# Optimization experiments

Measured on AMD Instinct MI355X. Metric: run time of the kernel, lower is better.

Reference implementation:

```python
import jax, jax.numpy as jnp
import numpy as np

NUM_HEADS = 8


def _nearest_idx(x, x_grid):
    # x: [b,n,dx]; x_grid: [b,H,W,dx] regular grid -> flat nearest cell index [b,n]
    b = x.shape[0]
    H, W = x_grid.shape[1], x_grid.shape[2]
    gf = x_grid.reshape(b, H * W, -1)
    lo = gf[:, :1]   # min corner [b,1,dx]
    hi = gf[:, -1:]  # max corner [b,1,dx]
    dims = jnp.asarray([H, W], dtype=x.dtype)
    t = (x - lo) / (hi - lo) * (dims - 1.0)
    idx = jnp.clip(jnp.round(t), 0.0, dims - 1.0).astype(jnp.int32)  # [b,n,2]
    return idx[..., 0] * W + idx[..., 1]


def _cumcount(idx):
    # per-batch cumulative count of each value, in order of appearance
    b, n = idx.shape
    order = jnp.argsort(idx, axis=1, stable=True)
    s = jnp.take_along_axis(idx, order, axis=1)
    ar = jnp.arange(n)
    new_run = jnp.concatenate([jnp.ones((b, 1), bool), s[:, 1:] != s[:, :-1]], axis=1)
    run_start = jax.lax.cummax(jnp.where(new_run, ar, 0), axis=1)
    cc_sorted = (ar - run_start).astype(jnp.int32)
    return jnp.zeros((b, n), jnp.int32).at[jnp.arange(b)[:, None], order].set(cc_sorted)


def _mhca(q_in, kv, mask, Wq, Wk, Wv, Wo):
    # q_in: [B,1,e]; kv: [B,K,e]; mask: [B,K] (True = attend)
    B, K, e = kv.shape
    dh = e // NUM_HEADS
    q = (q_in @ Wq).reshape(B, 1, NUM_HEADS, dh)
    k = (kv @ Wk).reshape(B, K, NUM_HEADS, dh)
    v = (kv @ Wv).reshape(B, K, NUM_HEADS, dh)
    scores = jnp.einsum('bqhd,bkhd->bhqk', q, k) / jnp.sqrt(jnp.asarray(dh, q.dtype))
    scores = jnp.where(mask[:, None, None, :], scores, jnp.finfo(scores.dtype).min)
    attn = jax.nn.softmax(scores, axis=-1)
    out = jnp.einsum('bhqk,bkhd->bqhd', attn, v).reshape(B, 1, e)
    return out @ Wo


def setup_inputs() -> dict:
    key = jax.random.key(0)
    ks = jax.random.split(key, 8)
    b, n, e, H, W = 8, 8192, 128, 64, 64
    x = jax.random.uniform(ks[0], (b, n, 2), jnp.float32)
    z = jax.random.normal(ks[1], (b, n, e), jnp.float32)
    g0 = jnp.linspace(0.0, 1.0, H)
    g1 = jnp.linspace(0.0, 1.0, W)
    mg = jnp.stack(jnp.meshgrid(g0, g1, indexing='ij'), axis=-1)  # [H,W,2]
    x_grid = jnp.broadcast_to(mg, (b, H, W, 2)).astype(jnp.float32)
    z_grid = jax.random.normal(ks[2], (b, H, W, e), jnp.float32)
    latent = jax.random.normal(ks[3], (e,), jnp.float32)
    scale = 1.0 / np.sqrt(e).astype(np.float32)
    Wq = jax.random.normal(ks[4], (e, e), jnp.float32) * scale
    Wk = jax.random.normal(ks[5], (e, e), jnp.float32) * scale
    Wv = jax.random.normal(ks[6], (e, e), jnp.float32) * scale
    Wo = jax.random.normal(ks[7], (e, e), jnp.float32) * scale
    return {"x": x, "z": z, "x_grid": x_grid, "z_grid": z_grid, "latent": latent,
            "Wq": Wq, "Wk": Wk, "Wv": Wv, "Wo": Wo, "max_patch": 20}


def reference(x, z, x_grid, z_grid, latent, Wq, Wk, Wv, Wo, max_patch):
    b, n, e = z.shape
    H, W = x_grid.shape[1], x_grid.shape[2]
    S = H * W
    nearest = _nearest_idx(x, x_grid)                    # [b,n]
    cc = _cumcount(nearest)                              # [b,n]
    bidx = jnp.broadcast_to(jnp.arange(b)[:, None], (b, n))
    valid = cc < max_patch
    slot = jnp.where(valid, cc, 0)
    # ragged scatter: pack each point's z into its grid cell's padded sequence
    joint = jnp.zeros((b, S, max_patch, e), z.dtype)
    joint = joint.at[bidx, nearest, slot].add(z * valid[..., None].astype(z.dtype))
    zg_flat = z_grid.reshape(b, S, e)
    joint = jnp.concatenate([joint, zg_flat[:, :, None, :]], axis=2)  # [b,S,P+1,e]
    counts = jnp.zeros((b, S), jnp.int32).at[bidx, nearest].add(1)
    mask = jnp.arange(max_patch + 1)[None, None, :] < jnp.minimum(counts, max_patch)[..., None]
    mask = mask.at[..., -1].set(True)  # grid token always attended
    joint = joint.reshape(b * S, max_patch + 1, e)
    mask = mask.reshape(b * S, max_patch + 1)
    q = jnp.broadcast_to(latent, (b * S, 1, e))          # z0_grid queries
    zg = _mhca(q, joint, mask, Wq, Wk, Wv, Wo)           # [b*S,1,e]
    zg = zg.reshape(b, H, W, e)
    return x_grid, zg
```

## Files before the change

kernel.cpp:

```cpp
#include <hip/hip_runtime.h>
#include <cstdint>
#include <cstddef>

#define S_CELLS 4096
#define NB      8
#define NPTS    8192
#define E       128
#define MAXP    20
#define NHEADS  8
#define NPT_ROWS 65536
#define NGR_ROWS 32768

#define WS_COUNTS 0
#define WS_SLOTS  131072
#define WS_WT1    2752512
#define WS_WT2    2793472
#define WS_SC     2828288
#define WS_V      5974016

typedef __attribute__((ext_vector_type(8))) short bf16x8;
typedef __attribute__((ext_vector_type(4))) float f32x4;

__device__ __forceinline__ unsigned short f2bf_bits(float f) {
    unsigned u = __float_as_uint(f);
    unsigned rounded = u + 0x7FFFu + ((u >> 16) & 1u);
    return (unsigned short)(rounded >> 16);
}
__device__ __forceinline__ unsigned short f2bf_rta(float f) {
    return (unsigned short)((__float_as_uint(f) + 0x8000u) >> 16);
}
__device__ __forceinline__ unsigned pack_bf2(float a, float b) {
    unsigned ua = __float_as_uint(a) + 0x8000u;
    unsigned ub = __float_as_uint(b) + 0x8000u;
    return (ua >> 16) | (ub & 0xFFFF0000u);
}
__device__ __forceinline__ float bf2f(unsigned short u) {
    return __uint_as_float(((unsigned)u) << 16);
}

__global__ void __launch_bounds__(256)
k_prep(const float* __restrict__ latent,
       const float* __restrict__ Wq,
       const float* __restrict__ Wk,
       const float* __restrict__ Wv,
       const float* __restrict__ Wo,
       int* __restrict__ counts,
       unsigned short* __restrict__ WT1,
       unsigned short* __restrict__ WT2) {
    const int t   = threadIdx.x;
    const int blk = blockIdx.x;

    {
        int4* c4 = (int4*)counts;
        for (int idx = blk * 256 + t; idx < 8192; idx += 9 * 256)
            c4[idx] = int4{0, 0, 0, 0};
    }

    if (blk == 0) {
        __shared__ float lat[E];
        __shared__ float qv[E];
        const int j = t & 127;
        if (t < E) lat[t] = latent[t];
        __syncthreads();
        float acc = 0.0f;
        for (int k2 = 0; k2 < E; ++k2) acc += lat[k2] * Wq[k2 * E + j];
        qv[j] = acc;
        __syncthreads();
        const int hb = (t >> 7) * 4;
        for (int h = hb; h < hb + 4; ++h) {
            float a = 0.0f;
            #pragma unroll
            for (int d = 0; d < 16; ++d) a += Wk[j * E + h * 16 + d] * qv[h * 16 + d];
            WT1[(size_t)(128 + h) * 136 + j] = f2bf_bits(a * 0.25f);
        }
        for (int idx = t; idx < 8 * 136; idx += 256) {
            int rr = idx / 136, cc = idx - rr * 136;
            WT1[(size_t)(136 + rr) * 136 + cc] = 0;
        }
        return;
    }

    const float* W = (blk < 5) ? Wv : Wo;
    unsigned short* WT = (blk < 5) ? WT1 : WT2;
    const int n0 = ((blk - 1) & 3) * 32;
    __shared__ float lbuf[128][33];
    #pragma unroll
    for (int it = 0; it < 16; ++it) {
        int k  = (t >> 5) + it * 8;
        int nl = t & 31;
        lbuf[k][nl] = W[(size_t)k * E + n0 + nl];
    }
    __syncthreads();
    for (int idx = t; idx < 32 * 136; idx += 256) {
        int nl = idx / 136, k = idx - nl * 136;
        float v = (k < 128) ? lbuf[k][nl] : 0.0f;
        WT[(size_t)(n0 + nl) * 136 + k] = f2bf_bits(v);
    }
}

__device__ __forceinline__ bf16x8 load_afrag_f32(const float* __restrict__ X,
                                                 int row, int kq, int q) {
    const float4* xr = (const float4*)(X + (size_t)row * E);
    float4 lo = xr[kq * 8 + q * 2];
    float4 hi = xr[kq * 8 + q * 2 + 1];
    unsigned u[4];
    u[0] = pack_bf2(lo.x, lo.y);
    u[1] = pack_bf2(lo.z, lo.w);
    u[2] = pack_bf2(hi.x, hi.y);
    u[3] = pack_bf2(hi.z, hi.w);
    union { unsigned u4[4]; bf16x8 v; } cv;
    cv.u4[0] = u[0]; cv.u4[1] = u[1]; cv.u4[2] = u[2]; cv.u4[3] = u[3];
    return cv.v;
}

__global__ void __launch_bounds__(256)
k_main(const float* __restrict__ x,
       const float* __restrict__ x_grid,
       const float* __restrict__ Xz,
       const float* __restrict__ Xg,
       const unsigned short* __restrict__ WT1g,
       int* __restrict__ counts,
       int* __restrict__ slots,
       unsigned short* __restrict__ V,
       float* __restrict__ SC,
       float* __restrict__ out_xgrid) {
    __shared__ unsigned short W_t[20480];

    const int t = threadIdx.x;

    if (blockIdx.x >= 768) {
        int i = (blockIdx.x - 768) * 256 + t;
        out_xgrid[i] = x_grid[i];
        int b = i >> 13;
        float x0 = x[(size_t)i * 2 + 0];
        float x1 = x[(size_t)i * 2 + 1];
        int i0 = (int)rintf(x0 * 63.0f);
        int i1 = (int)rintf(x1 * 63.0f);
        i0 = min(max(i0, 0), 63);
        i1 = min(max(i1, 0), 63);
        int cell = b * S_CELLS + i0 * 64 + i1;
        int slot = atomicAdd(&counts[cell], 1);
        if (slot < MAXP) slots[(size_t)cell * MAXP + slot] = i & (NPTS - 1);
        return;
    }

    {
        const float4* src = (const float4*)WT1g;
        float4* dst = (float4*)W_t;
        #pragma unroll
        for (int it = 0; it < 10; ++it) dst[t + it * 256] = src[t + it * 256];
    }
    __syncthreads();

    const int lane = t & 63;
    const int wv   = t >> 6;
    const int cn   = lane & 15;
    const int q    = lane >> 4;

    const int grow0 = blockIdx.x * 128;
    const float* Xsrc;
    int srow;
    if (blockIdx.x < 512) { Xsrc = Xz; srow = grow0; }
    else                  { Xsrc = Xg; srow = grow0 - NPT_ROWS; }

    f32x4 acc[2][9];
    #pragma unroll
    for (int mt = 0; mt < 2; ++mt)
        #pragma unroll
        for (int nt = 0; nt < 9; ++nt)
            acc[mt][nt] = f32x4{0.0f, 0.0f, 0.0f, 0.0f};

    #pragma unroll
    for (int kq = 0; kq < 4; ++kq) {
        bf16x8 a[2];
        #pragma unroll
        for (int mt = 0; mt < 2; ++mt)
            a[mt] = load_afrag_f32(Xsrc, srow + wv * 32 + mt * 16 + cn, kq, q);
        #pragma unroll
        for (int nt = 0; nt < 9; ++nt) {
            const bf16x8 b = *(const bf16x8*)&W_t[(size_t)(nt * 16 + cn) * 136 + kq * 32 + q * 8];
            #pragma unroll
            for (int mt = 0; mt < 2; ++mt)
                acc[mt][nt] = __builtin_amdgcn_mfma_f32_16x16x32_bf16(
                    a[mt], b, acc[mt][nt], 0, 0, 0);
        }
    }

    #pragma unroll
    for (int mt = 0; mt < 2; ++mt) {
        const int rb = grow0 + wv * 32 + mt * 16 + q * 4;
        #pragma unroll
        for (int nt = 0; nt < 8; ++nt)
            #pragma unroll
            for (int r = 0; r < 4; ++r)
                V[(size_t)(rb + r) * E + nt * 16 + cn] = f2bf_rta(acc[mt][nt][r]);
        if (cn < 8) {
            #pragma unroll
            for (int r = 0; r < 4; ++r)
                SC[(size_t)(rb + r) * NHEADS + cn] = acc[mt][8][r];
        }
    }
}

__global__ void __launch_bounds__(1024)
k_attn_proj(const int* __restrict__ counts,
            const int* __restrict__ slots,
            const float* __restrict__ SC,
            const unsigned short* __restrict__ Vg,
            const unsigned short* __restrict__ WT2g,
            float* __restrict__ zg) {
    __shared__ __align__(16) unsigned short X_s[16][136];

    const int t    = threadIdx.x;
    const int lane = t & 63;
    const int wv   = t >> 6;
    const int cb   = blockIdx.x * 16;
    const int b    = cb >> 12;
    const int base = b * NPTS;
    const int cn   = lane & 15;
    const int q    = lane >> 4;

    bf16x8 bfr[4];
    if (wv < 8) {
        #pragma unroll
        for (int kq = 0; kq < 4; ++kq)
            bfr[kq] = *(const bf16x8*)&WT2g[(size_t)(wv * 16 + cn) * 136 + kq * 32 + q * 8];
    }

    const int cell = cb + wv;
    const int m    = min(counts[cell], MAXP);
    int sl = (lane < MAXP) ? slots[(size_t)cell * MAXP + lane] : 0;
    const int h = lane >> 3;

    size_t r0 = (size_t)(NPT_ROWS + cell);
    float mm = SC[r0 * NHEADS + h];
    float ss = 1.0f;
    unsigned v0 = *(const unsigned*)(Vg + r0 * E + 2 * lane);
    float o0 = bf2f((unsigned short)v0);
    float o1 = bf2f((unsigned short)(v0 >> 16));

    for (int t0 = 0; t0 < m; t0 += 4) {
        float av[4], p0[4], p1[4];
        #pragma unroll
        for (int j = 0; j < 4; ++j) {
            int pt = __shfl(sl, t0 + j, 64);
            bool val = (t0 + j) < m;
            pt = val ? pt : 0;
            size_t r = (size_t)(base + pt);
            float sa = SC[r * NHEADS + h];
            av[j] = val ? sa : -1e30f;
            unsigned vv = *(const unsigned*)(Vg + r * E + 2 * lane);
            p0[j] = bf2f((unsigned short)vv);
            p1[j] = bf2f((unsigned short)(vv >> 16));
        }
        #pragma unroll
        for (int j = 0; j < 4; ++j) {
            float nm = fmaxf(mm, av[j]);
            float e  = __expf(av[j] - nm);
            float al = __expf(mm - nm);
            ss = ss * al + e;
            o0 = o0 * al + e * p0[j];
            o1 = o1 * al + e * p1[j];
            mm = nm;
        }
    }
    float inv = 1.0f / ss;
    *(unsigned*)&X_s[wv][2 * lane] = pack_bf2(o0 * inv, o1 * inv);
    __syncthreads();

    if (wv < 8) {
        f32x4 acc = f32x4{0.0f, 0.0f, 0.0f, 0.0f};
        #pragma unroll
        for (int kq = 0; kq < 4; ++kq) {
            bf16x8 a = *(const bf16x8*)&X_s[cn][kq * 32 + q * 8];
            acc = __builtin_amdgcn_mfma_f32_16x16x32_bf16(a, bfr[kq], acc, 0, 0, 0);
        }
        #pragma unroll
        for (int r = 0; r < 4; ++r)
            zg[(size_t)(cb + q * 4 + r) * E + wv * 16 + cn] = acc[r];
    }
}

extern "C" void kernel_launch(void* const* d_in, const int* in_sizes, int n_in,
                              void* d_out, int out_size, void* d_ws, size_t ws_size,
                              hipStream_t stream) {
    const float* x      = (const float*)d_in[0];
    const float* z      = (const float*)d_in[1];
    const float* x_grid = (const float*)d_in[2];
    const float* z_grid = (const float*)d_in[3];
    const float* latent = (const float*)d_in[4];
    const float* Wq     = (const float*)d_in[5];
    const float* Wk     = (const float*)d_in[6];
    const float* Wv     = (const float*)d_in[7];
    const float* Wo     = (const float*)d_in[8];

    char* ws = (char*)d_ws;
    int*            counts = (int*)(ws + WS_COUNTS);
    int*            slots  = (int*)(ws + WS_SLOTS);
    unsigned short* WT1    = (unsigned short*)(ws + WS_WT1);
    unsigned short* WT2    = (unsigned short*)(ws + WS_WT2);
    float*          SC     = (float*)(ws + WS_SC);
    unsigned short* V      = (unsigned short*)(ws + WS_V);

    float* out_xgrid = (float*)d_out;
    float* zg        = (float*)d_out + NB * NPTS;

    k_prep<<<9, 256, 0, stream>>>(latent, Wq, Wk, Wv, Wo, counts, WT1, WT2);

    k_main<<<1024, 256, 0, stream>>>(x, x_grid, z, z_grid, WT1,
                                     counts, slots, V, SC, out_xgrid);

    k_attn_proj<<<2048, 1024, 0, stream>>>(counts, slots, SC, V, WT2, zg);
}
```

Measured before the change: 137.0 us.

## Fuse weight prep into main kernel and bin points per batch in shared memory

Removes the separate prep kernel launch. Each GEMM block now builds its own bf16 transposed Wv tile and the folded q·Wk rows in shared memory, and a few extra blocks prepare WT2 and copy x_grid with float4 stores. Point binning becomes one block per batch using shared-memory atomic counters and writes counts at the end, so the global count zeroing and global atomics go away. The trade-off is redundant per-block weight conversion and the q projection, plus serialised binning over 8192 points in each of 8 blocks, which may sit on the critical path.

```diff
diff --git a/kernel.cpp b/kernel.cpp
--- a/kernel.cpp
+++ b/kernel.cpp
@@ -13,7 +13,6 @@
 
 #define WS_COUNTS 0
 #define WS_SLOTS  131072
-#define WS_WT1    2752512
 #define WS_WT2    2793472
 #define WS_SC     2828288
 #define WS_V      5974016
@@ -34,68 +33,11 @@
     unsigned ub = __float_as_uint(b) + 0x8000u;
     return (ua >> 16) | (ub & 0xFFFF0000u);
 }
+__device__ __forceinline__ unsigned pack_bf2_rne(float a, float b) {
+    return ((unsigned)f2bf_bits(a)) | (((unsigned)f2bf_bits(b)) << 16);
+}
 __device__ __forceinline__ float bf2f(unsigned short u) {
     return __uint_as_float(((unsigned)u) << 16);
-}
-
-__global__ void __launch_bounds__(256)
-k_prep(const float* __restrict__ latent,
-       const float* __restrict__ Wq,
-       const float* __restrict__ Wk,
-       const float* __restrict__ Wv,
-       const float* __restrict__ Wo,
-       int* __restrict__ counts,
-       unsigned short* __restrict__ WT1,
-       unsigned short* __restrict__ WT2) {
-    const int t   = threadIdx.x;
-    const int blk = blockIdx.x;
-
-    {
-        int4* c4 = (int4*)counts;
-        for (int idx = blk * 256 + t; idx < 8192; idx += 9 * 256)
-            c4[idx] = int4{0, 0, 0, 0};
-    }
-
-    if (blk == 0) {
-        __shared__ float lat[E];
-        __shared__ float qv[E];
-        const int j = t & 127;
-        if (t < E) lat[t] = latent[t];
-        __syncthreads();
-        float acc = 0.0f;
-        for (int k2 = 0; k2 < E; ++k2) acc += lat[k2] * Wq[k2 * E + j];
-        qv[j] = acc;
-        __syncthreads();
-        const int hb = (t >> 7) * 4;
-        for (int h = hb; h < hb + 4; ++h) {
-            float a = 0.0f;
-            #pragma unroll
-            for (int d = 0; d < 16; ++d) a += Wk[j * E + h * 16 + d] * qv[h * 16 + d];
-            WT1[(size_t)(128 + h) * 136 + j] = f2bf_bits(a * 0.25f);
-        }
-        for (int idx = t; idx < 8 * 136; idx += 256) {
-            int rr = idx / 136, cc = idx - rr * 136;
-            WT1[(size_t)(136 + rr) * 136 + cc] = 0;
-        }
-        return;
-    }
-
-    const float* W = (blk < 5) ? Wv : Wo;
-    unsigned short* WT = (blk < 5) ? WT1 : WT2;
-    const int n0 = ((blk - 1) & 3) * 32;
-    __shared__ float lbuf[128][33];
-    #pragma unroll
-    for (int it = 0; it < 16; ++it) {
-        int k  = (t >> 5) + it * 8;
-        int nl = t & 31;
-        lbuf[k][nl] = W[(size_t)k * E + n0 + nl];
-    }
-    __syncthreads();
-    for (int idx = t; idx < 32 * 136; idx += 256) {
-        int nl = idx / 136, k = idx - nl * 136;
-        float v = (k < 128) ? lbuf[k][nl] : 0.0f;
-        WT[(size_t)(n0 + nl) * 136 + k] = f2bf_bits(v);
-    }
 }
 
 __device__ __forceinline__ bf16x8 load_afrag_f32(const float* __restrict__ X,
@@ -114,41 +56,109 @@
 }
 
 __global__ void __launch_bounds__(256)
-k_main(const float* __restrict__ x,
-       const float* __restrict__ x_grid,
-       const float* __restrict__ Xz,
-       const float* __restrict__ Xg,
-       const unsigned short* __restrict__ WT1g,
-       int* __restrict__ counts,
-       int* __restrict__ slots,
-       unsigned short* __restrict__ V,
-       float* __restrict__ SC,
-       float* __restrict__ out_xgrid) {
-    __shared__ unsigned short W_t[20480];
-
-    const int t = threadIdx.x;
-
-    if (blockIdx.x >= 768) {
-        int i = (blockIdx.x - 768) * 256 + t;
-        out_xgrid[i] = x_grid[i];
-        int b = i >> 13;
-        float x0 = x[(size_t)i * 2 + 0];
-        float x1 = x[(size_t)i * 2 + 1];
-        int i0 = (int)rintf(x0 * 63.0f);
-        int i1 = (int)rintf(x1 * 63.0f);
-        i0 = min(max(i0, 0), 63);
-        i1 = min(max(i1, 0), 63);
-        int cell = b * S_CELLS + i0 * 64 + i1;
-        int slot = atomicAdd(&counts[cell], 1);
-        if (slot < MAXP) slots[(size_t)cell * MAXP + slot] = i & (NPTS - 1);
+k_fused(const float* __restrict__ x,
+        const float* __restrict__ x_grid,
+        const float* __restrict__ Xz,
+        const float* __restrict__ Xg,
+        const float* __restrict__ latent,
+        const float* __restrict__ Wq,
+        const float* __restrict__ Wk,
+        const float* __restrict__ Wv,
+        const float* __restrict__ Wo,
+        int* __restrict__ counts,
+        int* __restrict__ slots,
+        unsigned short* __restrict__ V,
+        float* __restrict__ SC,
+        unsigned short* __restrict__ WT2,
+        float* __restrict__ out_xgrid) {
+    __shared__ __align__(16) char smem[40192];
+    const int t   = threadIdx.x;
+    const int blk = blockIdx.x;
+
+    if (blk >= 768) {
+        if (blk < 776) {
+            int* lcnt = (int*)smem;
+            const int b = blk - 768;
+            for (int i = t; i < S_CELLS; i += 256) lcnt[i] = 0;
+            __syncthreads();
+            const float2* xp = (const float2*)x;
+            const size_t base = (size_t)b * NPTS;
+            #pragma unroll 2
+            for (int r = 0; r < NPTS; r += 256) {
+                int p = r + t;
+                float2 xv = xp[base + p];
+                int i0 = (int)rintf(xv.x * 63.0f);
+                int i1 = (int)rintf(xv.y * 63.0f);
+                i0 = min(max(i0, 0), 63);
+                i1 = min(max(i1, 0), 63);
+                int cl = i0 * 64 + i1;
+                int slot = atomicAdd(&lcnt[cl], 1);
+                if (slot < MAXP)
+                    slots[(size_t)(b * S_CELLS + cl) * MAXP + slot] = p;
+            }
+            __syncthreads();
+            for (int i = t; i < S_CELLS; i += 256)
+                counts[b * S_CELLS + i] = lcnt[i];
+        } else if (blk < 780) {
+            float (*lbuf)[33] = (float(*)[33])smem;
+            const int n0 = (blk - 776) * 32;
+            #pragma unroll
+            for (int it = 0; it < 16; ++it) {
+                int k  = (t >> 5) + it * 8;
+                int nl = t & 31;
+                lbuf[k][nl] = Wo[(size_t)k * E + n0 + nl];
+            }
+            __syncthreads();
+            for (int idx = t; idx < 32 * 136; idx += 256) {
+                int nl = idx / 136, k = idx - nl * 136;
+                float v = (k < 128) ? lbuf[k][nl] : 0.0f;
+                WT2[(size_t)(n0 + nl) * 136 + k] = f2bf_bits(v);
+            }
+        } else {
+            int idx = (blk - 780) * 256 + t;
+            ((float4*)out_xgrid)[idx] = ((const float4*)x_grid)[idx];
+        }
         return;
     }
 
+    unsigned short* W_t = (unsigned short*)smem;
+    float* lat = (float*)(smem + 39168);
+    float* qv  = (float*)(smem + 39680);
+
+    if (t < E) lat[t] = latent[t];
+
+    #pragma unroll 8
+    for (int it = 0; it < 32; ++it) {
+        int idx = t + it * 256;
+        int kp  = idx >> 7;
+        int n   = idx & 127;
+        float a = Wv[(size_t)(2 * kp)     * E + n];
+        float b = Wv[(size_t)(2 * kp + 1) * E + n];
+        *(unsigned*)&W_t[(size_t)n * 136 + 2 * kp] = pack_bf2_rne(a, b);
+    }
+    for (int idx = t; idx < 8 * 136; idx += 256) {
+        int rr = idx / 136, cc = idx - rr * 136;
+        W_t[(size_t)(136 + rr) * 136 + cc] = 0;
+    }
+    __syncthreads();
+
+    if (t < E) {
+        float acc = 0.0f;
+        for (int k2 = 0; k2 < E; ++k2) acc += lat[k2] * Wq[k2 * E + t];
+        qv[t] = acc;
+    }
+    __syncthreads();
+
     {
-        const float4* src = (const float4*)WT1g;
-        float4* dst = (float4*)W_t;
-        #pragma unroll
-        for (int it = 0; it < 10; ++it) dst[t + it * 256] = src[t + it * 256];
+        const int j  = t & 127;
+        const int hb = (t >> 7) * 4;
+        for (int h = hb; h < hb + 4; ++h) {
+            float a = 0.0f;
+            #pragma unroll
+            for (int d = 0; d < 16; ++d)
+                a += Wk[j * E + h * 16 + d] * qv[h * 16 + d];
+            W_t[(size_t)(128 + h) * 136 + j] = f2bf_bits(a * 0.25f);
+        }
     }
     __syncthreads();
 
@@ -157,11 +167,11 @@
     const int cn   = lane & 15;
     const int q    = lane >> 4;
 
-    const int grow0 = blockIdx.x * 128;
+    const int grow0 = blk * 128;
     const float* Xsrc;
     int srow;
-    if (blockIdx.x < 512) { Xsrc = Xz; srow = grow0; }
-    else                  { Xsrc = Xg; srow = grow0 - NPT_ROWS; }
+    if (blk < 512) { Xsrc = Xz; srow = grow0; }
+    else           { Xsrc = Xg; srow = grow0 - NPT_ROWS; }
 
     f32x4 acc[2][9];
     #pragma unroll
@@ -297,7 +307,6 @@
     char* ws = (char*)d_ws;
     int*            counts = (int*)(ws + WS_COUNTS);
     int*            slots  = (int*)(ws + WS_SLOTS);
-    unsigned short* WT1    = (unsigned short*)(ws + WS_WT1);
     unsigned short* WT2    = (unsigned short*)(ws + WS_WT2);
     float*          SC     = (float*)(ws + WS_SC);
     unsigned short* V      = (unsigned short*)(ws + WS_V);
@@ -305,10 +314,9 @@
     float* out_xgrid = (float*)d_out;
     float* zg        = (float*)d_out + NB * NPTS;
 
-    k_prep<<<9, 256, 0, stream>>>(latent, Wq, Wk, Wv, Wo, counts, WT1, WT2);
-
-    k_main<<<1024, 256, 0, stream>>>(x, x_grid, z, z_grid, WT1,
-                                     counts, slots, V, SC, out_xgrid);
+    k_fused<<<844, 256, 0, stream>>>(x, x_grid, z, z_grid, latent,
+                                     Wq, Wk, Wv, Wo,
+                                     counts, slots, V, SC, WT2, out_xgrid);
 
     k_attn_proj<<<2048, 1024, 0, stream>>>(counts, slots, SC, V, WT2, zg);
 }
```

Measured after the change: 156.4 us. 1.14x slower.

## Defer V projection: aggregate raw z per head, then project after attention

Applied to the files above, without the earlier changes.

The main kernel now computes only the attention score columns instead of also projecting every point and grid row through Wv and storing a bf16 V buffer. The attention kernel gathers raw fp32 z rows, forms per-head softmax-weighted sums of them, and applies the Wv projection per head with MFMA on the aggregated rows before the Wo projection. This removes the large V write and read, at the cost of reading fp32 z (twice the bytes per gathered row), eight per-head accumulators per lane, and an extra matmul stage per cell. The online softmax is also replaced by a two-pass max/sum over at most 21 tokens.

```diff
diff --git a/kernel.cpp b/kernel.cpp
--- a/kernel.cpp
+++ b/kernel.cpp
@@ -16,7 +16,6 @@
 #define WS_WT1    2752512
 #define WS_WT2    2793472
 #define WS_SC     2828288
-#define WS_V      5974016
 
 typedef __attribute__((ext_vector_type(8))) short bf16x8;
 typedef __attribute__((ext_vector_type(4))) float f32x4;
@@ -33,9 +32,6 @@
     unsigned ua = __float_as_uint(a) + 0x8000u;
     unsigned ub = __float_as_uint(b) + 0x8000u;
     return (ua >> 16) | (ub & 0xFFFF0000u);
-}
-__device__ __forceinline__ float bf2f(unsigned short u) {
-    return __uint_as_float(((unsigned)u) << 16);
 }
 
 __global__ void __launch_bounds__(256)
@@ -121,10 +117,9 @@
        const unsigned short* __restrict__ WT1g,
        int* __restrict__ counts,
        int* __restrict__ slots,
-       unsigned short* __restrict__ V,
        float* __restrict__ SC,
        float* __restrict__ out_xgrid) {
-    __shared__ unsigned short W_t[20480];
+    __shared__ __align__(16) unsigned short sA[16 * 136];
 
     const int t = threadIdx.x;
 
@@ -145,10 +140,9 @@
     }
 
     {
-        const float4* src = (const float4*)WT1g;
-        float4* dst = (float4*)W_t;
-        #pragma unroll
-        for (int it = 0; it < 10; ++it) dst[t + it * 256] = src[t + it * 256];
+        const float4* src = (const float4*)(WT1g + 128 * 136);
+        float4* dst = (float4*)sA;
+        if (t < 272) dst[t] = src[t];
     }
     __syncthreads();
 
@@ -163,121 +157,140 @@
     if (blockIdx.x < 512) { Xsrc = Xz; srow = grow0; }
     else                  { Xsrc = Xg; srow = grow0 - NPT_ROWS; }
 
-    f32x4 acc[2][9];
-    #pragma unroll
-    for (int mt = 0; mt < 2; ++mt)
-        #pragma unroll
-        for (int nt = 0; nt < 9; ++nt)
-            acc[mt][nt] = f32x4{0.0f, 0.0f, 0.0f, 0.0f};
+    f32x4 acc[2];
+    acc[0] = f32x4{0.0f, 0.0f, 0.0f, 0.0f};
+    acc[1] = f32x4{0.0f, 0.0f, 0.0f, 0.0f};
 
     #pragma unroll
     for (int kq = 0; kq < 4; ++kq) {
-        bf16x8 a[2];
-        #pragma unroll
-        for (int mt = 0; mt < 2; ++mt)
-            a[mt] = load_afrag_f32(Xsrc, srow + wv * 32 + mt * 16 + cn, kq, q);
-        #pragma unroll
-        for (int nt = 0; nt < 9; ++nt) {
-            const bf16x8 b = *(const bf16x8*)&W_t[(size_t)(nt * 16 + cn) * 136 + kq * 32 + q * 8];
-            #pragma unroll
-            for (int mt = 0; mt < 2; ++mt)
-                acc[mt][nt] = __builtin_amdgcn_mfma_f32_16x16x32_bf16(
-                    a[mt], b, acc[mt][nt], 0, 0, 0);
+        const bf16x8 b = *(const bf16x8*)&sA[cn * 136 + kq * 32 + q * 8];
+        #pragma unroll
+        for (int mt = 0; mt < 2; ++mt) {
+            bf16x8 a = load_afrag_f32(Xsrc, srow + wv * 32 + mt * 16 + cn, kq, q);
+            acc[mt] = __builtin_amdgcn_mfma_f32_16x16x32_bf16(b, a, acc[mt], 0, 0, 0);
         }
     }
 
     #pragma unroll
     for (int mt = 0; mt < 2; ++mt) {
-        const int rb = grow0 + wv * 32 + mt * 16 + q * 4;
-        #pragma unroll
-        for (int nt = 0; nt < 8; ++nt)
-            #pragma unroll
-            for (int r = 0; r < 4; ++r)
-                V[(size_t)(rb + r) * E + nt * 16 + cn] = f2bf_rta(acc[mt][nt][r]);
-        if (cn < 8) {
-            #pragma unroll
-            for (int r = 0; r < 4; ++r)
-                SC[(size_t)(rb + r) * NHEADS + cn] = acc[mt][8][r];
-        }
-    }
-}
-
-__global__ void __launch_bounds__(1024)
+        const int rb = grow0 + wv * 32 + mt * 16 + cn;
+        if (q < 2)
+            *(f32x4*)(SC + (size_t)rb * NHEADS + q * 4) = acc[mt];
+    }
+}
+
+__global__ void __launch_bounds__(512)
 k_attn_proj(const int* __restrict__ counts,
             const int* __restrict__ slots,
             const float* __restrict__ SC,
-            const unsigned short* __restrict__ Vg,
+            const float* __restrict__ Xz,
+            const float* __restrict__ Zg,
+            const unsigned short* __restrict__ WT1g,
             const unsigned short* __restrict__ WT2g,
             float* __restrict__ zg) {
+    __shared__ __align__(16) unsigned short Y_s[8][16][136];
     __shared__ __align__(16) unsigned short X_s[16][136];
 
     const int t    = threadIdx.x;
     const int lane = t & 63;
     const int wv   = t >> 6;
-    const int cb   = blockIdx.x * 16;
-    const int b    = cb >> 12;
+    const int cb   = blockIdx.x * 8;
+    const int cell = cb + wv;
+    const int b    = cell >> 12;
     const int base = b * NPTS;
     const int cn   = lane & 15;
     const int q    = lane >> 4;
 
-    bf16x8 bfr[4];
-    if (wv < 8) {
-        #pragma unroll
-        for (int kq = 0; kq < 4; ++kq)
-            bfr[kq] = *(const bf16x8*)&WT2g[(size_t)(wv * 16 + cn) * 136 + kq * 32 + q * 8];
-    }
-
-    const int cell = cb + wv;
-    const int m    = min(counts[cell], MAXP);
+    const int m = min(counts[cell], MAXP);
     int sl = (lane < MAXP) ? slots[(size_t)cell * MAXP + lane] : 0;
-    const int h = lane >> 3;
-
-    size_t r0 = (size_t)(NPT_ROWS + cell);
-    float mm = SC[r0 * NHEADS + h];
-    float ss = 1.0f;
-    unsigned v0 = *(const unsigned*)(Vg + r0 * E + 2 * lane);
-    float o0 = bf2f((unsigned short)v0);
-    float o1 = bf2f((unsigned short)(v0 >> 16));
-
-    for (int t0 = 0; t0 < m; t0 += 4) {
-        float av[4], p0[4], p1[4];
+
+    const int hh = lane & 7;
+    const int tb = lane >> 3;
+
+    float sarr[3];
+    #pragma unroll
+    for (int p = 0; p < 3; ++p) {
+        int tt = tb + 8 * p;
+        int pt = __shfl(sl, tt, 64);
+        bool isPt = tt < m;
+        bool isG  = tt == m;
+        size_t r = isG ? (size_t)(NPT_ROWS + cell)
+                       : (size_t)(base + (isPt ? pt : 0));
+        float sc = SC[r * NHEADS + hh];
+        sarr[p] = (isPt || isG) ? sc : -1e30f;
+    }
+    float mx = fmaxf(fmaxf(sarr[0], sarr[1]), sarr[2]);
+    mx = fmaxf(mx, __shfl_xor(mx, 8, 64));
+    mx = fmaxf(mx, __shfl_xor(mx, 16, 64));
+    mx = fmaxf(mx, __shfl_xor(mx, 32, 64));
+    float e0 = __expf(sarr[0] - mx);
+    float e1 = __expf(sarr[1] - mx);
+    float e2 = __expf(sarr[2] - mx);
+    float sum = e0 + e1 + e2;
+    sum += __shfl_xor(sum, 8, 64);
+    sum += __shfl_xor(sum, 16, 64);
+    sum += __shfl_xor(sum, 32, 64);
+    float inv = 1.0f / sum;
+    float wn0 = e0 * inv, wn1 = e1 * inv, wn2 = e2 * inv;
+
+    float y0[8], y1[8];
+    #pragma unroll
+    for (int h2 = 0; h2 < 8; ++h2) { y0[h2] = 0.0f; y1[h2] = 0.0f; }
+
+    const int ntok = m + 1;
+    for (int t0 = 0; t0 < ntok; t0 += 4) {
+        float wnp = (t0 < 8) ? wn0 : ((t0 < 16) ? wn1 : wn2);
+        float2 zv[4];
         #pragma unroll
         for (int j = 0; j < 4; ++j) {
-            int pt = __shfl(sl, t0 + j, 64);
-            bool val = (t0 + j) < m;
-            pt = val ? pt : 0;
-            size_t r = (size_t)(base + pt);
-            float sa = SC[r * NHEADS + h];
-            av[j] = val ? sa : -1e30f;
-            unsigned vv = *(const unsigned*)(Vg + r * E + 2 * lane);
-            p0[j] = bf2f((unsigned short)vv);
-            p1[j] = bf2f((unsigned short)(vv >> 16));
+            int tt = t0 + j;
+            int pt = __shfl(sl, tt, 64);
+            const float* zr = (tt == m)
+                ? (Zg + (size_t)cell * E)
+                : (Xz + (size_t)(base + ((tt < m) ? pt : 0)) * E);
+            zv[j] = *(const float2*)(zr + 2 * lane);
         }
         #pragma unroll
         for (int j = 0; j < 4; ++j) {
-            float nm = fmaxf(mm, av[j]);
-            float e  = __expf(av[j] - nm);
-            float al = __expf(mm - nm);
-            ss = ss * al + e;
-            o0 = o0 * al + e * p0[j];
-            o1 = o1 * al + e * p1[j];
-            mm = nm;
-        }
-    }
-    float inv = 1.0f / ss;
-    *(unsigned*)&X_s[wv][2 * lane] = pack_bf2(o0 * inv, o1 * inv);
+            int srcb = ((t0 + j) & 7) << 3;
+            #pragma unroll
+            for (int h2 = 0; h2 < 8; ++h2) {
+                float w = __shfl(wnp, srcb + h2, 64);
+                y0[h2] = fmaf(w, zv[j].x, y0[h2]);
+                y1[h2] = fmaf(w, zv[j].y, y1[h2]);
+            }
+        }
+    }
+
+    #pragma unroll
+    for (int h2 = 0; h2 < 8; ++h2)
+        *(unsigned*)&Y_s[h2][wv][2 * lane] = pack_bf2(y0[h2], y1[h2]);
     __syncthreads();
 
-    if (wv < 8) {
-        f32x4 acc = f32x4{0.0f, 0.0f, 0.0f, 0.0f};
+    {
+        f32x4 acc2 = f32x4{0.0f, 0.0f, 0.0f, 0.0f};
         #pragma unroll
         for (int kq = 0; kq < 4; ++kq) {
-            bf16x8 a = *(const bf16x8*)&X_s[cn][kq * 32 + q * 8];
-            acc = __builtin_amdgcn_mfma_f32_16x16x32_bf16(a, bfr[kq], acc, 0, 0, 0);
+            bf16x8 aY = *(const bf16x8*)&Y_s[wv][cn][kq * 32 + q * 8];
+            bf16x8 bW = *(const bf16x8*)&WT1g[(size_t)(wv * 16 + cn) * 136 + kq * 32 + q * 8];
+            acc2 = __builtin_amdgcn_mfma_f32_16x16x32_bf16(aY, bW, acc2, 0, 0, 0);
         }
         #pragma unroll
         for (int r = 0; r < 4; ++r)
-            zg[(size_t)(cb + q * 4 + r) * E + wv * 16 + cn] = acc[r];
+            X_s[q * 4 + r][wv * 16 + cn] = f2bf_rta(acc2[r]);
+    }
+    __syncthreads();
+
+    {
+        f32x4 acc3 = f32x4{0.0f, 0.0f, 0.0f, 0.0f};
+        #pragma unroll
+        for (int kq = 0; kq < 4; ++kq) {
+            bf16x8 a   = *(const bf16x8*)&X_s[cn][kq * 32 + q * 8];
+            bf16x8 bfr = *(const bf16x8*)&WT2g[(size_t)(wv * 16 + cn) * 136 + kq * 32 + q * 8];
+            acc3 = __builtin_amdgcn_mfma_f32_16x16x32_bf16(bfr, a, acc3, 0, 0, 0);
+        }
+        if (cn < 8)
+            *(f32x4*)(zg + (size_t)(cb + cn) * E + wv * 16 + q * 4) = acc3;
     }
 }
 
@@ -300,7 +313,6 @@
     unsigned short* WT1    = (unsigned short*)(ws + WS_WT1);
     unsigned short* WT2    = (unsigned short*)(ws + WS_WT2);
     float*          SC     = (float*)(ws + WS_SC);
-    unsigned short* V      = (unsigned short*)(ws + WS_V);
 
     float* out_xgrid = (float*)d_out;
     float* zg        = (float*)d_out + NB * NPTS;
@@ -308,7 +320,8 @@
     k_prep<<<9, 256, 0, stream>>>(latent, Wq, Wk, Wv, Wo, counts, WT1, WT2);
 
     k_main<<<1024, 256, 0, stream>>>(x, x_grid, z, z_grid, WT1,
-                                     counts, slots, V, SC, out_xgrid);
-
-    k_attn_proj<<<2048, 1024, 0, stream>>>(counts, slots, SC, V, WT2, zg);
-}
+                                     counts, slots, SC, out_xgrid);
+
+    k_attn_proj<<<4096, 512, 0, stream>>>(counts, slots, SC, z, z_grid,
+                                          WT1, WT2, zg);
+}
```

Result: slower. 156.1 us (+14.0%).
